# Performance work log

Measured on AMD Instinct MI355X. Metric: run time of the kernel, lower is better.

## Reference

```python
import jax, jax.numpy as jnp
import numpy as np

REG = 0.1
N_ITER = 10
EPS = 1e-8


def setup_inputs() -> dict:
    key = jax.random.key(0)
    k1, k2 = jax.random.split(key)
    B, L_S, L_T, D = 8, 1024, 1024, 768
    return {
        "student_tokens": jax.random.normal(k1, (B, L_S, D), dtype=jnp.float32),
        "teacher_tokens": jax.random.normal(k2, (B, L_T, D), dtype=jnp.float32),
    }


def reference(student_tokens, teacher_tokens):
    B, L_S, _ = student_tokens.shape
    L_T = teacher_tokens.shape[1]
    # Euclidean cdist via ||x||^2 + ||y||^2 - 2<x,y>, clamped, sqrt  -> (B, L_S, L_T)
    sq_s = jnp.sum(student_tokens * student_tokens, axis=-1)  # (B, L_S)
    sq_t = jnp.sum(teacher_tokens * teacher_tokens, axis=-1)  # (B, L_T)
    inner = jnp.einsum("bsd,btd->bst", student_tokens, teacher_tokens)
    C = jnp.sqrt(jnp.maximum(sq_s[:, :, None] + sq_t[:, None, :] - 2.0 * inner, 0.0))
    a = jnp.full((B, L_S), 1.0 / L_S, dtype=C.dtype)
    b = jnp.full((B, L_T), 1.0 / L_T, dtype=C.dtype)
    K = jnp.exp(-C / REG)
    u = jnp.ones_like(a)
    v = jnp.ones_like(b)
    for _ in range(N_ITER):  # fixed small iteration count, unrolled
        v = b / (jnp.einsum("bst,bs->bt", K, u) + EPS)
        u = a / (jnp.einsum("bst,bt->bs", K, v) + EPS)
    P = u[:, :, None] * K * v[:, None, :]
    return jnp.sum(P * C, axis=(1, 2)).mean()
```

## Files before the change

kernel.cpp:

```cpp
#include <hip/hip_runtime.h>
#include <hip/hip_bf16.h>

#define B_   8
#define LS_  1024
#define LT_  1024
#define D_   768
#define INV_REG 10.0f
#define EPS_ 1e-8f
#define AVAL (1.0f/1024.0f)
#define BVAL (1.0f/1024.0f)
#define NITER 10
#define IBLK 512
#define RPB  16

typedef __attribute__((ext_vector_type(8))) short bf16x8;
typedef __attribute__((ext_vector_type(4))) float f32x4;

__device__ inline unsigned short f2bf(float f) {
    __hip_bfloat16 h = __float2bfloat16(f);
    return __builtin_bit_cast(unsigned short, h);
}
__device__ inline float bf2f(unsigned short u) {
    unsigned int x = ((unsigned int)u) << 16;
    return __builtin_bit_cast(float, x);
}

__global__ __launch_bounds__(256) void init_bufs(float* partialB, float* out) {
    int i = threadIdx.x;
    if (i < B_) partialB[i] = 0.0f;
    if (i == 0) out[0] = 0.0f;
}

__global__ __launch_bounds__(192) void prep_rows(const float* __restrict__ S, const float* __restrict__ T,
                                                 unsigned short* __restrict__ sbf, unsigned short* __restrict__ tbf,
                                                 float* __restrict__ sqS, float* __restrict__ sqT) {
    int bid = blockIdx.x;
    bool teach = bid >= B_*LS_;
    int row = teach ? bid - B_*LS_ : bid;
    const float* src = (teach ? T : S) + (size_t)row * D_;
    unsigned short* dst = (teach ? tbf : sbf) + (size_t)row * D_;
    int t = threadIdx.x;
    float4 v = *(const float4*)(src + t * 4);
    float ss = v.x*v.x + v.y*v.y + v.z*v.z + v.w*v.w;
    ushort4 o;
    o.x = f2bf(v.x); o.y = f2bf(v.y); o.z = f2bf(v.z); o.w = f2bf(v.w);
    *(ushort4*)(dst + t * 4) = o;
    for (int off = 32; off; off >>= 1) ss += __shfl_down(ss, off);
    __shared__ float red[3];
    int wid = t >> 6, lane = t & 63;
    if (lane == 0) red[wid] = ss;
    __syncthreads();
    if (t == 0) (teach ? sqT : sqS)[row] = red[0] + red[1] + red[2];
}

__device__ inline void gload_lds16(const void* g, void* l) {
    __builtin_amdgcn_global_load_lds((const __attribute__((address_space(1))) void*)g,
                                     (__attribute__((address_space(3))) void*)l, 16, 0, 0);
}

__global__ __launch_bounds__(256) void gemm_cdist(const unsigned short* __restrict__ S,
                                                  const unsigned short* __restrict__ T,
                                                  const float* __restrict__ sqS, const float* __restrict__ sqT,
                                                  unsigned short* __restrict__ Kb,
                                                  unsigned short* __restrict__ Cbm) {
    __shared__ unsigned short As[128 * 32];
    __shared__ unsigned short Bs[128 * 32];
    const int bid  = blockIdx.x;
    const int b    = bid & 7;
    const int tile = bid >> 3;
    const int brow = (tile >> 3) * 128;
    const int bcol = (tile & 7) * 128;
    const int tid  = threadIdx.x;
    const int wid  = tid >> 6, lane = tid & 63;
    const int wr = wid >> 1, wc = wid & 1;
    const unsigned short* Sg = S + ((size_t)b * LS_ + brow) * D_;
    const unsigned short* Tg = T + ((size_t)b * LT_ + bcol) * D_;

    f32x4 acc[4][4] = {};
    const int r16 = lane & 15, kg = lane >> 4;

    for (int k0 = 0; k0 < D_; k0 += 32) {
        #pragma unroll
        for (int j = 0; j < 2; ++j) {
            int lin = j * 256 + tid;
            int row = lin >> 2, c8 = (lin & 3) * 8;
            unsigned short* la = As + (size_t)(j * 256 + wid * 64) * 8;
            unsigned short* lb = Bs + (size_t)(j * 256 + wid * 64) * 8;
            gload_lds16(Sg + (size_t)row * D_ + k0 + c8, la);
            gload_lds16(Tg + (size_t)row * D_ + k0 + c8, lb);
        }
        __syncthreads();
        bf16x8 af[4], bfr[4];
        #pragma unroll
        for (int f = 0; f < 4; ++f) {
            af[f]  = *(const bf16x8*)(As + (wr * 64 + f * 16 + r16) * 32 + kg * 8);
            bfr[f] = *(const bf16x8*)(Bs + (wc * 64 + f * 16 + r16) * 32 + kg * 8);
        }
        #pragma unroll
        for (int i = 0; i < 4; ++i)
            #pragma unroll
            for (int j = 0; j < 4; ++j)
                acc[i][j] = __builtin_amdgcn_mfma_f32_16x16x32_bf16(af[i], bfr[j], acc[i][j], 0, 0, 0);
        __syncthreads();
    }

    #pragma unroll
    for (int i = 0; i < 4; ++i) {
        int gr0 = brow + wr * 64 + i * 16 + (lane >> 4) * 4;
        #pragma unroll
        for (int j = 0; j < 4; ++j) {
            int gc = bcol + wc * 64 + j * 16 + (lane & 15);
            float st = sqT[b * LT_ + gc];
            #pragma unroll
            for (int r = 0; r < 4; ++r) {
                float ss = sqS[b * LS_ + gr0 + r];
                float d2 = ss + st - 2.0f * acc[i][j][r];
                float c  = sqrtf(fmaxf(d2, 0.0f));
                size_t idx = ((size_t)b << 20) + (size_t)(gr0 + r) * LT_ + gc;
                Kb[idx]  = f2bf(__expf(-INV_REG * c));
                Cbm[idx] = f2bf(c);
            }
        }
    }
}

__global__ __launch_bounds__(256) void prepass(const unsigned short* __restrict__ Kb,
                                               float* __restrict__ slab) {
    const int bid = blockIdx.x;
    const int b = bid & 7, blk = bid >> 3;
    const int s0 = blk * RPB;
    const int tid = threadIdx.x;
    const unsigned short* Kbat = Kb + ((size_t)b << 20);
    float a0 = 0.f, a1 = 0.f, a2 = 0.f, a3 = 0.f;
    #pragma unroll
    for (int r = 0; r < RPB; ++r) {
        ushort4 k4 = *(const ushort4*)(Kbat + ((size_t)(s0 + r) << 10) + tid * 4);
        a0 += bf2f(k4.x); a1 += bf2f(k4.y); a2 += bf2f(k4.z); a3 += bf2f(k4.w);
    }
    *(float4*)(slab + ((size_t)(b * 64 + blk) << 10) + tid * 4) = make_float4(a0, a1, a2, a3);
}

__global__ __launch_bounds__(256) void reduce_v(const float* __restrict__ slab,
                                                float* __restrict__ v) {
    const int b = blockIdx.x;
    const int tid = threadIdx.x;
    const float* base = slab + ((size_t)(b * 64) << 10) + tid * 4;
    float4 acc = make_float4(0.f, 0.f, 0.f, 0.f);
    #pragma unroll 8
    for (int p = 0; p < 64; ++p) {
        float4 s = *(const float4*)(base + ((size_t)p << 10));
        acc.x += s.x; acc.y += s.y; acc.z += s.z; acc.w += s.w;
    }
    float4 o;
    o.x = BVAL / (acc.x + EPS_);
    o.y = BVAL / (acc.y + EPS_);
    o.z = BVAL / (acc.z + EPS_);
    o.w = BVAL / (acc.w + EPS_);
    *(float4*)(v + (b << 10) + tid * 4) = o;
}

__global__ __launch_bounds__(256) void sink_iter(const unsigned short* __restrict__ Kb,
                                                 const float* __restrict__ v,
                                                 float* __restrict__ slab) {
    const int bid = blockIdx.x;
    const int b = bid & 7, blk = bid >> 3;
    const int s0 = blk * RPB;
    const int tid = threadIdx.x;
    const int w = tid >> 6, lane = tid & 63;
    const int c4 = lane * 4;
    const unsigned short* Kbat = Kb + ((size_t)b << 20);
    const float* vb = v + (b << 10);
    __shared__ float ush[RPB];

    float4 vq[4];
    #pragma unroll
    for (int q = 0; q < 4; ++q) vq[q] = *(const float4*)(vb + q * 256 + c4);
    #pragma unroll
    for (int rr = 0; rr < 4; ++rr) {
        int s = s0 + w * 4 + rr;
        const unsigned short* Kr = Kbat + ((size_t)s << 10);
        float acc = 0.f;
        #pragma unroll
        for (int q = 0; q < 4; ++q) {
            ushort4 k4 = *(const ushort4*)(Kr + q * 256 + c4);
            acc += bf2f(k4.x) * vq[q].x + bf2f(k4.y) * vq[q].y
                 + bf2f(k4.z) * vq[q].z + bf2f(k4.w) * vq[q].w;
        }
        for (int off = 32; off; off >>= 1) acc += __shfl_down(acc, off);
        if (lane == 0) ush[w * 4 + rr] = AVAL / (acc + EPS_);
    }
    __syncthreads();

    float a0 = 0.f, a1 = 0.f, a2 = 0.f, a3 = 0.f;
    #pragma unroll
    for (int r = 0; r < RPB; ++r) {
        float u = ush[r];
        ushort4 k4 = *(const ushort4*)(Kbat + ((size_t)(s0 + r) << 10) + tid * 4);
        a0 += bf2f(k4.x) * u; a1 += bf2f(k4.y) * u;
        a2 += bf2f(k4.z) * u; a3 += bf2f(k4.w) * u;
    }
    *(float4*)(slab + ((size_t)(b * 64 + blk) << 10) + tid * 4) = make_float4(a0, a1, a2, a3);
}

__global__ __launch_bounds__(256) void final_loss(const unsigned short* __restrict__ Kb,
                                                  const unsigned short* __restrict__ Cbm,
                                                  const float* __restrict__ v,
                                                  float* __restrict__ part) {
    const int bid = blockIdx.x;
    const int b = bid & 7, blk = bid >> 3;
    const int s0 = blk * RPB;
    const int tid = threadIdx.x;
    const int w = tid >> 6, lane = tid & 63;
    const int c4 = lane * 4;
    const unsigned short* Kbat = Kb + ((size_t)b << 20);
    const unsigned short* Cbat = Cbm + ((size_t)b << 20);
    const float* vb = v + (b << 10);

    float4 vq[4];
    #pragma unroll
    for (int q = 0; q < 4; ++q) vq[q] = *(const float4*)(vb + q * 256 + c4);
    float bacc = 0.f;
    #pragma unroll
    for (int rr = 0; rr < 4; ++rr) {
        int s = s0 + w * 4 + rr;
        const unsigned short* Kr = Kbat + ((size_t)s << 10);
        const unsigned short* Cr = Cbat + ((size_t)s << 10);
        float rk = 0.f, rkc = 0.f;
        #pragma unroll
        for (int q = 0; q < 4; ++q) {
            ushort4 k4 = *(const ushort4*)(Kr + q * 256 + c4);
            ushort4 cc = *(const ushort4*)(Cr + q * 256 + c4);
            float k0 = bf2f(k4.x) * vq[q].x, k1 = bf2f(k4.y) * vq[q].y;
            float k2 = bf2f(k4.z) * vq[q].z, k3 = bf2f(k4.w) * vq[q].w;
            rk  += k0 + k1 + k2 + k3;
            rkc += k0 * bf2f(cc.x) + k1 * bf2f(cc.y) + k2 * bf2f(cc.z) + k3 * bf2f(cc.w);
        }
        for (int off = 32; off; off >>= 1) {
            rk  += __shfl_down(rk, off);
            rkc += __shfl_down(rkc, off);
        }
        if (lane == 0) bacc += (AVAL / (rk + EPS_)) * rkc;
    }
    __shared__ float red[4];
    if (lane == 0) red[w] = bacc;
    __syncthreads();
    if (tid == 0) atomicAdd(&part[b], red[0] + red[1] + red[2] + red[3]);
}

__global__ void finalize(const float* __restrict__ partialB, float* __restrict__ out) {
    if (threadIdx.x == 0) {
        float s = 0.0f;
        for (int i = 0; i < B_; ++i) s += partialB[i];
        out[0] = s / (float)B_;
    }
}

extern "C" void kernel_launch(void* const* d_in, const int* in_sizes, int n_in,
                              void* d_out, int out_size, void* d_ws, size_t ws_size,
                              hipStream_t stream) {
    const float* S = (const float*)d_in[0];
    const float* T = (const float*)d_in[1];
    float* out = (float*)d_out;
    char* ws = (char*)d_ws;

    const size_t offKb   = 0;
    const size_t offCb   = offKb   + (size_t)B_*LS_*LT_*2;
    const size_t offSbf  = offCb   + (size_t)B_*LS_*LT_*2;
    const size_t offTbf  = offSbf  + (size_t)B_*LS_*D_*2;
    const size_t offSqS  = offTbf  + (size_t)B_*LT_*D_*2;
    const size_t offSqT  = offSqS  + (size_t)B_*LS_*4;
    const size_t offSlab = offSqT  + (size_t)B_*LT_*4;
    const size_t offV    = offSlab + (size_t)IBLK*LT_*4;
    const size_t offPart = offV    + (size_t)B_*LT_*4;
    const size_t need    = offPart + 64;
    if (ws_size < need) return;

    unsigned short* Kb  = (unsigned short*)(ws + offKb);
    unsigned short* Cbm = (unsigned short*)(ws + offCb);
    unsigned short* sbf = (unsigned short*)(ws + offSbf);
    unsigned short* tbf = (unsigned short*)(ws + offTbf);
    float* sqS  = (float*)(ws + offSqS);
    float* sqT  = (float*)(ws + offSqT);
    float* slab = (float*)(ws + offSlab);
    float* v    = (float*)(ws + offV);
    float* part = (float*)(ws + offPart);

    init_bufs<<<1, 256, 0, stream>>>(part, out);
    prep_rows<<<2 * B_ * LS_, 192, 0, stream>>>(S, T, sbf, tbf, sqS, sqT);
    gemm_cdist<<<512, 256, 0, stream>>>(sbf, tbf, sqS, sqT, Kb, Cbm);

    prepass<<<IBLK, 256, 0, stream>>>(Kb, slab);
    for (int i = 0; i < NITER - 1; ++i) {
        reduce_v<<<B_, 256, 0, stream>>>(slab, v);
        sink_iter<<<IBLK, 256, 0, stream>>>(Kb, v, slab);
    }
    reduce_v<<<B_, 256, 0, stream>>>(slab, v);
    final_loss<<<IBLK, 256, 0, stream>>>(Kb, Cbm, v, part);
    finalize<<<1, 64, 0, stream>>>(part, out);
}
```

Measured before the change: 211.6 us.

## Fuse v reduction into Sinkhorn iteration kernels with double-buffered slabs

Removes the separate 8-block reduce_v launches. Each sink_iter and final_loss block now sums the previous partial slabs into LDS itself, and ping-pong slab buffers avoid read/write hazards. Blocks cover 32 rows instead of 16, which halves the slab count. The final loss writes per-block partials that a 256-thread reduction kernel sums, replacing atomics and the init kernel. This cuts launches and the latency-bound serial reduction, at the cost of every block redundantly re-reading all partial slabs from cache.

New measurement: 200.8 us. 5.1% less time.

```diff
diff --git a/kernel.cpp b/kernel.cpp
--- a/kernel.cpp
+++ b/kernel.cpp
@@ -10,8 +10,9 @@
 #define AVAL (1.0f/1024.0f)
 #define BVAL (1.0f/1024.0f)
 #define NITER 10
-#define IBLK 512
-#define RPB  16
+#define IBLK 256
+#define BPB  32
+#define RPB  32
 
 typedef __attribute__((ext_vector_type(8))) short bf16x8;
 typedef __attribute__((ext_vector_type(4))) float f32x4;
@@ -23,12 +24,6 @@
 __device__ inline float bf2f(unsigned short u) {
     unsigned int x = ((unsigned int)u) << 16;
     return __builtin_bit_cast(float, x);
-}
-
-__global__ __launch_bounds__(256) void init_bufs(float* partialB, float* out) {
-    int i = threadIdx.x;
-    if (i < B_) partialB[i] = 0.0f;
-    if (i == 0) out[0] = 0.0f;
 }
 
 __global__ __launch_bounds__(192) void prep_rows(const float* __restrict__ S, const float* __restrict__ T,
@@ -132,36 +127,17 @@
     const int tid = threadIdx.x;
     const unsigned short* Kbat = Kb + ((size_t)b << 20);
     float a0 = 0.f, a1 = 0.f, a2 = 0.f, a3 = 0.f;
-    #pragma unroll
+    #pragma unroll 8
     for (int r = 0; r < RPB; ++r) {
         ushort4 k4 = *(const ushort4*)(Kbat + ((size_t)(s0 + r) << 10) + tid * 4);
         a0 += bf2f(k4.x); a1 += bf2f(k4.y); a2 += bf2f(k4.z); a3 += bf2f(k4.w);
     }
-    *(float4*)(slab + ((size_t)(b * 64 + blk) << 10) + tid * 4) = make_float4(a0, a1, a2, a3);
-}
-
-__global__ __launch_bounds__(256) void reduce_v(const float* __restrict__ slab,
-                                                float* __restrict__ v) {
-    const int b = blockIdx.x;
-    const int tid = threadIdx.x;
-    const float* base = slab + ((size_t)(b * 64) << 10) + tid * 4;
-    float4 acc = make_float4(0.f, 0.f, 0.f, 0.f);
-    #pragma unroll 8
-    for (int p = 0; p < 64; ++p) {
-        float4 s = *(const float4*)(base + ((size_t)p << 10));
-        acc.x += s.x; acc.y += s.y; acc.z += s.z; acc.w += s.w;
-    }
-    float4 o;
-    o.x = BVAL / (acc.x + EPS_);
-    o.y = BVAL / (acc.y + EPS_);
-    o.z = BVAL / (acc.z + EPS_);
-    o.w = BVAL / (acc.w + EPS_);
-    *(float4*)(v + (b << 10) + tid * 4) = o;
+    *(float4*)(slab + ((size_t)(b * BPB + blk) << 10) + tid * 4) = make_float4(a0, a1, a2, a3);
 }
 
 __global__ __launch_bounds__(256) void sink_iter(const unsigned short* __restrict__ Kb,
-                                                 const float* __restrict__ v,
-                                                 float* __restrict__ slab) {
+                                                 const float* __restrict__ src,
+                                                 float* __restrict__ dst) {
     const int bid = blockIdx.x;
     const int b = bid & 7, blk = bid >> 3;
     const int s0 = blk * RPB;
@@ -169,15 +145,30 @@
     const int w = tid >> 6, lane = tid & 63;
     const int c4 = lane * 4;
     const unsigned short* Kbat = Kb + ((size_t)b << 20);
-    const float* vb = v + (b << 10);
+    __shared__ float v_lds[1024];
     __shared__ float ush[RPB];
 
+    {
+        const float* base = src + ((size_t)(b * BPB) << 10) + tid * 4;
+        float4 acc = make_float4(0.f, 0.f, 0.f, 0.f);
+        #pragma unroll 8
+        for (int p = 0; p < BPB; ++p) {
+            float4 s = *(const float4*)(base + ((size_t)p << 10));
+            acc.x += s.x; acc.y += s.y; acc.z += s.z; acc.w += s.w;
+        }
+        v_lds[tid * 4 + 0] = BVAL / (acc.x + EPS_);
+        v_lds[tid * 4 + 1] = BVAL / (acc.y + EPS_);
+        v_lds[tid * 4 + 2] = BVAL / (acc.z + EPS_);
+        v_lds[tid * 4 + 3] = BVAL / (acc.w + EPS_);
+    }
+    __syncthreads();
+
     float4 vq[4];
     #pragma unroll
-    for (int q = 0; q < 4; ++q) vq[q] = *(const float4*)(vb + q * 256 + c4);
-    #pragma unroll
-    for (int rr = 0; rr < 4; ++rr) {
-        int s = s0 + w * 4 + rr;
+    for (int q = 0; q < 4; ++q) vq[q] = *(const float4*)&v_lds[q * 256 + c4];
+    #pragma unroll
+    for (int rr = 0; rr < 8; ++rr) {
+        int s = s0 + w * 8 + rr;
         const unsigned short* Kr = Kbat + ((size_t)s << 10);
         float acc = 0.f;
         #pragma unroll
@@ -187,25 +178,25 @@
                  + bf2f(k4.z) * vq[q].z + bf2f(k4.w) * vq[q].w;
         }
         for (int off = 32; off; off >>= 1) acc += __shfl_down(acc, off);
-        if (lane == 0) ush[w * 4 + rr] = AVAL / (acc + EPS_);
+        if (lane == 0) ush[w * 8 + rr] = AVAL / (acc + EPS_);
     }
     __syncthreads();
 
     float a0 = 0.f, a1 = 0.f, a2 = 0.f, a3 = 0.f;
-    #pragma unroll
+    #pragma unroll 8
     for (int r = 0; r < RPB; ++r) {
         float u = ush[r];
         ushort4 k4 = *(const ushort4*)(Kbat + ((size_t)(s0 + r) << 10) + tid * 4);
         a0 += bf2f(k4.x) * u; a1 += bf2f(k4.y) * u;
         a2 += bf2f(k4.z) * u; a3 += bf2f(k4.w) * u;
     }
-    *(float4*)(slab + ((size_t)(b * 64 + blk) << 10) + tid * 4) = make_float4(a0, a1, a2, a3);
+    *(float4*)(dst + ((size_t)(b * BPB + blk) << 10) + tid * 4) = make_float4(a0, a1, a2, a3);
 }
 
 __global__ __launch_bounds__(256) void final_loss(const unsigned short* __restrict__ Kb,
                                                   const unsigned short* __restrict__ Cbm,
-                                                  const float* __restrict__ v,
-                                                  float* __restrict__ part) {
+                                                  const float* __restrict__ src,
+                                                  float* __restrict__ partial) {
     const int bid = blockIdx.x;
     const int b = bid & 7, blk = bid >> 3;
     const int s0 = blk * RPB;
@@ -214,15 +205,30 @@
     const int c4 = lane * 4;
     const unsigned short* Kbat = Kb + ((size_t)b << 20);
     const unsigned short* Cbat = Cbm + ((size_t)b << 20);
-    const float* vb = v + (b << 10);
+    __shared__ float v_lds[1024];
+
+    {
+        const float* base = src + ((size_t)(b * BPB) << 10) + tid * 4;
+        float4 acc = make_float4(0.f, 0.f, 0.f, 0.f);
+        #pragma unroll 8
+        for (int p = 0; p < BPB; ++p) {
+            float4 s = *(const float4*)(base + ((size_t)p << 10));
+            acc.x += s.x; acc.y += s.y; acc.z += s.z; acc.w += s.w;
+        }
+        v_lds[tid * 4 + 0] = BVAL / (acc.x + EPS_);
+        v_lds[tid * 4 + 1] = BVAL / (acc.y + EPS_);
+        v_lds[tid * 4 + 2] = BVAL / (acc.z + EPS_);
+        v_lds[tid * 4 + 3] = BVAL / (acc.w + EPS_);
+    }
+    __syncthreads();
 
     float4 vq[4];
     #pragma unroll
-    for (int q = 0; q < 4; ++q) vq[q] = *(const float4*)(vb + q * 256 + c4);
+    for (int q = 0; q < 4; ++q) vq[q] = *(const float4*)&v_lds[q * 256 + c4];
     float bacc = 0.f;
     #pragma unroll
-    for (int rr = 0; rr < 4; ++rr) {
-        int s = s0 + w * 4 + rr;
+    for (int rr = 0; rr < 8; ++rr) {
+        int s = s0 + w * 8 + rr;
         const unsigned short* Kr = Kbat + ((size_t)s << 10);
         const unsigned short* Cr = Cbat + ((size_t)s << 10);
         float rk = 0.f, rkc = 0.f;
@@ -244,15 +250,18 @@
     __shared__ float red[4];
     if (lane == 0) red[w] = bacc;
     __syncthreads();
-    if (tid == 0) atomicAdd(&part[b], red[0] + red[1] + red[2] + red[3]);
-}
-
-__global__ void finalize(const float* __restrict__ partialB, float* __restrict__ out) {
-    if (threadIdx.x == 0) {
-        float s = 0.0f;
-        for (int i = 0; i < B_; ++i) s += partialB[i];
-        out[0] = s / (float)B_;
-    }
+    if (tid == 0) partial[bid] = red[0] + red[1] + red[2] + red[3];
+}
+
+__global__ __launch_bounds__(256) void finalize(const float* __restrict__ partial, float* __restrict__ out) {
+    int tid = threadIdx.x;
+    float x = partial[tid];
+    for (int off = 32; off; off >>= 1) x += __shfl_down(x, off);
+    __shared__ float red[4];
+    int w = tid >> 6, lane = tid & 63;
+    if (lane == 0) red[w] = x;
+    __syncthreads();
+    if (tid == 0) out[0] = (red[0] + red[1] + red[2] + red[3]) / (float)B_;
 }
 
 extern "C" void kernel_launch(void* const* d_in, const int* in_sizes, int n_in,
@@ -269,10 +278,10 @@
     const size_t offTbf  = offSbf  + (size_t)B_*LS_*D_*2;
     const size_t offSqS  = offTbf  + (size_t)B_*LT_*D_*2;
     const size_t offSqT  = offSqS  + (size_t)B_*LS_*4;
-    const size_t offSlab = offSqT  + (size_t)B_*LT_*4;
-    const size_t offV    = offSlab + (size_t)IBLK*LT_*4;
-    const size_t offPart = offV    + (size_t)B_*LT_*4;
-    const size_t need    = offPart + 64;
+    const size_t offSlabA= offSqT  + (size_t)B_*LT_*4;
+    const size_t offSlabB= offSlabA+ (size_t)IBLK*LT_*4;
+    const size_t offPart = offSlabB+ (size_t)IBLK*LT_*4;
+    const size_t need    = offPart + IBLK*4;
     if (ws_size < need) return;
 
     unsigned short* Kb  = (unsigned short*)(ws + offKb);
@@ -281,20 +290,19 @@
     unsigned short* tbf = (unsigned short*)(ws + offTbf);
     float* sqS  = (float*)(ws + offSqS);
     float* sqT  = (float*)(ws + offSqT);
-    float* slab = (float*)(ws + offSlab);
-    float* v    = (float*)(ws + offV);
+    float* slabA= (float*)(ws + offSlabA);
+    float* slabB= (float*)(ws + offSlabB);
     float* part = (float*)(ws + offPart);
 
-    init_bufs<<<1, 256, 0, stream>>>(part, out);
     prep_rows<<<2 * B_ * LS_, 192, 0, stream>>>(S, T, sbf, tbf, sqS, sqT);
     gemm_cdist<<<512, 256, 0, stream>>>(sbf, tbf, sqS, sqT, Kb, Cbm);
 
-    prepass<<<IBLK, 256, 0, stream>>>(Kb, slab);
+    prepass<<<IBLK, 256, 0, stream>>>(Kb, slabA);
+    float* cur = slabA; float* nxt = slabB;
     for (int i = 0; i < NITER - 1; ++i) {
-        reduce_v<<<B_, 256, 0, stream>>>(slab, v);
-        sink_iter<<<IBLK, 256, 0, stream>>>(Kb, v, slab);
-    }
-    reduce_v<<<B_, 256, 0, stream>>>(slab, v);
-    final_loss<<<IBLK, 256, 0, stream>>>(Kb, Cbm, v, part);
-    finalize<<<1, 64, 0, stream>>>(part, out);
-}
+        sink_iter<<<IBLK, 256, 0, stream>>>(Kb, cur, nxt);
+        float* t2 = cur; cur = nxt; nxt = t2;
+    }
+    final_loss<<<IBLK, 256, 0, stream>>>(Kb, Cbm, cur, part);
+    finalize<<<1, IBLK, 0, stream>>>(part, out);
+}
```
